# Optimization experiments

Hardware: AMD Instinct MI355X
Metric: run time of the kernel (lower is better)

## Reference

```python
import jax, jax.numpy as jnp
import numpy as np

B, C, H, W = 4, 64, 96, 96
O = 64          # out_channel
K = 9           # 3x3 kernel positions
PAD = 1


def conv3x3(x, w, b):
    # NCHW 3x3 conv, stride 1, pad 1
    y = jax.lax.conv_general_dilated(
        x, w, window_strides=(1, 1), padding=((PAD, PAD), (PAD, PAD)),
        dimension_numbers=("NCHW", "OIHW", "NCHW"))
    return y + b[None, :, None, None]


def deform_conv3x3(x, offset, w, b):
    """torchvision-style DeformConv2d, 3x3, stride 1, pad 1, 1 offset group.
    x: [B, Cin, H, W]; offset: [B, 2*K, H, W] ordered (dy, dx) per kernel pos.
    """
    Bb, Cin, Hh, Ww = x.shape
    off = offset.reshape(Bb, K, 2, Hh, Ww)
    ky, kx = jnp.meshgrid(jnp.arange(3), jnp.arange(3), indexing="ij")
    ky = ky.reshape(K).astype(x.dtype)
    kx = kx.reshape(K).astype(x.dtype)
    hh = jnp.arange(Hh, dtype=x.dtype)
    ww = jnp.arange(Ww, dtype=x.dtype)
    # sampling coords: p0 + p_k + delta_p  -> [B, K, H, W]
    py = hh[None, None, :, None] - PAD + ky[None, :, None, None] + off[:, :, 0]
    px = ww[None, None, None, :] - PAD + kx[None, :, None, None] + off[:, :, 1]

    y0 = jnp.floor(py).astype(jnp.int32)
    x0 = jnp.floor(px).astype(jnp.int32)
    dy = py - y0.astype(x.dtype)
    dx = px - x0.astype(x.dtype)

    x_flat = x.reshape(Bb, Cin, Hh * Ww)

    def gather(yi, xi, wgt):
        valid = ((yi >= 0) & (yi < Hh) & (xi >= 0) & (xi < Ww)).astype(x.dtype)
        idx = (jnp.clip(yi, 0, Hh - 1) * Ww + jnp.clip(xi, 0, Ww - 1)).reshape(Bb, -1)
        vals = jax.vmap(lambda xf, ix: xf[:, ix])(x_flat, idx)  # [B, Cin, K*H*W]
        return vals * (wgt * valid).reshape(Bb, 1, -1)

    sampled = (gather(y0,     x0,     (1 - dy) * (1 - dx))
             + gather(y0,     x0 + 1, (1 - dy) * dx)
             + gather(y0 + 1, x0,     dy * (1 - dx))
             + gather(y0 + 1, x0 + 1, dy * dx))
    sampled = sampled.reshape(Bb, Cin, K, Hh, Ww)
    out = jnp.einsum("bckhw,ock->bohw", sampled, w.reshape(O, Cin, K))
    return out + b[None, :, None, None]


def setup_inputs() -> dict:
    key = jax.random.key(0)
    ks = jax.random.split(key, 6)
    ref_feat = jax.random.normal(ks[0], (B, C, H, W), dtype=jnp.float32)
    dist_feat = jax.random.normal(ks[1], (B, C, H, W), dtype=jnp.float32)
    offset_w = jax.random.normal(ks[2], (2 * K, C, 3, 3), dtype=jnp.float32) * 0.01
    offset_b = jnp.zeros((2 * K,), dtype=jnp.float32)
    deform_w = jax.random.normal(ks[3], (O, 3 * C, 3, 3), dtype=jnp.float32) * 0.05
    deform_b = jax.random.normal(ks[4], (O,), dtype=jnp.float32) * 0.05
    return {"ref_feat": ref_feat, "dist_feat": dist_feat,
            "offset_w": offset_w, "offset_b": offset_b,
            "deform_w": deform_w, "deform_b": deform_b}


def reference(ref_feat, dist_feat, offset_w, offset_b, deform_w, deform_b):
    offset = conv3x3(ref_feat, offset_w, offset_b)
    diff = (ref_feat - dist_feat) ** 2
    feat_in = jnp.concatenate((ref_feat, dist_feat, diff), axis=1)  # [B, 3C, H, W]
    feat = deform_conv3x3(feat_in, offset, deform_w, deform_b)
    feat = jax.nn.relu(feat)
    return (feat, diff)
```

## Files before the change

### kernel.cpp

```cpp
#include <hip/hip_runtime.h>
#include <hip/hip_fp16.h>

#define Wd    96
#define Hd    96
#define HW    9216
#define Bn    4
#define Cn    64
#define C3    192
#define On    64
#define NPIX  (Bn*HW)
#define NFEAT (Bn*Cn*HW)
#define NWTB  (9*6*4*512)
#define NWTB2 (18*2*64*8)
#define NRB3  (Bn*(HW/32))

#define HR    5
#define HC    21
#define HPITCH 400
#define NPR   (HR*HC)

typedef __attribute__((ext_vector_type(8))) short s8v;
typedef __attribute__((ext_vector_type(8))) _Float16 h8v;
typedef __attribute__((ext_vector_type(4))) unsigned int u4v;
typedef __attribute__((ext_vector_type(4))) float f4v;

__device__ __forceinline__ unsigned packh(float lo, float hi) {
    __half2 h = __floats2half2_rn(lo, hi);
    return __builtin_bit_cast(unsigned, h);
}

__global__ __launch_bounds__(256) void repack_wts_kernel(
        const float* __restrict__ ref,
        const float* __restrict__ dist,
        unsigned int* __restrict__ packed,
        float* __restrict__ out_diff,
        const float* __restrict__ dw,
        const float* __restrict__ ow,
        __half* __restrict__ wtb,
        __half* __restrict__ wtb2) {
    __shared__ unsigned lds[96][33];

    int tid = threadIdx.x;

    if (blockIdx.x >= NRB3) {
        int e = (int)(blockIdx.x - NRB3) * 256 + tid;
        if (e < NWTB) {
            int j = e & 7;
            int L = (e >> 3) & 63;
            int mt = (e >> 9) & 3;
            int rest = e >> 11;
            int kc = rest % 6;
            int tap = rest / 6;
            int o = mt * 16 + (L & 15);
            int c = kc * 32 + (L >> 4) * 8 + j;
            wtb[e] = __float2half(dw[((size_t)o * C3 + c) * 9 + tap]);
        } else if (e < NWTB + NWTB2) {
            int e2 = e - NWTB;
            int j = e2 & 7;
            int L = (e2 >> 3) & 63;
            int mt = (e2 >> 9) & 1;
            int kc2 = e2 >> 10;
            int v = mt * 16 + (L & 15);
            int k = kc2 * 32 + ((L >> 4) & 3) * 8 + j;
            int c = k & 63;
            int tap = k >> 6;
            float val = (v < 18) ? ow[((size_t)v * Cn + c) * 9 + tap] : 0.f;
            wtb2[e2] = __float2half(val);
        }
        return;
    }

    int blk = blockIdx.x;
    int b = blk / (HW / 32);
    int pb = (blk - b * (HW / 32)) * 32;
    int pxg = tid & 7;
    int chp = tid >> 3;

    size_t base0 = ((size_t)(b * Cn + 2 * chp)) * HW + pb + pxg * 4;
    size_t base1 = base0 + HW;

    f4v r0 = *(const f4v*)(ref + base0);
    f4v r1 = *(const f4v*)(ref + base1);
    f4v d0 = *(const f4v*)(dist + base0);
    f4v d1 = *(const f4v*)(dist + base1);

    f4v q0 = (r0 - d0) * (r0 - d0);
    f4v q1 = (r1 - d1) * (r1 - d1);
    *(f4v*)(out_diff + base0) = q0;
    *(f4v*)(out_diff + base1) = q1;

#pragma unroll
    for (int j = 0; j < 4; ++j) {
        int p = pxg * 4 + j;
        lds[chp][p]      = packh(r0[j], r1[j]);
        lds[32 + chp][p] = packh(d0[j], d1[j]);
        lds[64 + chp][p] = packh(q0[j], q1[j]);
    }
    __syncthreads();

    unsigned* pko = packed + (size_t)(b * HW + pb) * 96;
#pragma unroll
    for (int k = 0; k < 12; ++k) {
        int i = tid + k * 256;
        int p = i / 96;
        int cp = i - p * 96;
        pko[p * 96 + cp] = lds[cp][p];
    }
}

struct Ctx {
    int o00, o01, o10, o11;
    int l00, l01, l10, l11;
    float W00, W01, W10, W11;
    int inh;
};

__device__ __forceinline__ Ctx mkctx(int t, int y, int x, int xb, float2 o2) {
    Ctx c;
    float py = (float)(y - 1 + t / 3) + o2.x;
    float pxs = (float)(x - 1 + t % 3) + o2.y;
    float fy = floorf(py), fx = floorf(pxs);
    int y0 = (int)fy, x0 = (int)fx;
    int y1 = y0 + 1, x1 = x0 + 1;
    float ay = py - fy, ax = pxs - fx;
    bool vy0 = (unsigned)y0 < (unsigned)Hd;
    bool vy1 = (unsigned)y1 < (unsigned)Hd;
    bool vx0 = (unsigned)x0 < (unsigned)Wd;
    bool vx1 = (unsigned)x1 < (unsigned)Wd;
    c.W00 = (vy0 && vx0) ? (1.f - ay) * (1.f - ax) : 0.f;
    c.W01 = (vy0 && vx1) ? (1.f - ay) * ax : 0.f;
    c.W10 = (vy1 && vx0) ? ay * (1.f - ax) : 0.f;
    c.W11 = (vy1 && vx1) ? ay * ax : 0.f;
    int y0c = min(max(y0, 0), Hd - 1), y1c = min(max(y1, 0), Hd - 1);
    int x0c = min(max(x0, 0), Wd - 1), x1c = min(max(x1, 0), Wd - 1);
    c.o00 = (y0c * Wd + x0c) * (C3 * 2);
    c.o01 = (y0c * Wd + x1c) * (C3 * 2);
    c.o10 = (y1c * Wd + x0c) * (C3 * 2);
    c.o11 = (y1c * Wd + x1c) * (C3 * 2);
    int iy0 = y0c - y + 2, iy1 = y1c - y + 2;
    int ix0 = x0c - xb + 3, ix1 = x1c - xb + 3;
    c.inh = ((unsigned)iy0 < (unsigned)HR) & ((unsigned)iy1 < (unsigned)HR) &
            ((unsigned)ix0 < (unsigned)HC) & ((unsigned)ix1 < (unsigned)HC);
    c.l00 = (iy0 * HC + ix0) * HPITCH;
    c.l01 = (iy0 * HC + ix1) * HPITCH;
    c.l10 = (iy1 * HC + ix0) * HPITCH;
    c.l11 = (iy1 * HC + ix1) * HPITCH;
    return c;
}

__device__ __forceinline__ __half2 uh2(unsigned u) {
    return __builtin_bit_cast(__half2, u);
}

__device__ __forceinline__ void bilin_mfma(const s8v* rw, const Ctx& cc,
        const s8v* __restrict__ Ap, int t, int kb, int L, f4v* acc) {
    __half2 w00 = __float2half2_rn(cc.W00);
    __half2 w01 = __float2half2_rn(cc.W01);
    __half2 w10 = __float2half2_rn(cc.W10);
    __half2 w11 = __float2half2_rn(cc.W11);
#pragma unroll
    for (int i = 0; i < 3; ++i) {
        int kc = kb + i;
        u4v u00 = __builtin_bit_cast(u4v, rw[0 * 3 + i]);
        u4v u01 = __builtin_bit_cast(u4v, rw[1 * 3 + i]);
        u4v u10 = __builtin_bit_cast(u4v, rw[2 * 3 + i]);
        u4v u11 = __builtin_bit_cast(u4v, rw[3 * 3 + i]);
        u4v bu;
#pragma unroll
        for (int p = 0; p < 4; ++p) {
            __half2 v = __hmul2(uh2(u00[p]), w00);
            v = __hfma2(uh2(u01[p]), w01, v);
            v = __hfma2(uh2(u10[p]), w10, v);
            v = __hfma2(uh2(u11[p]), w11, v);
            bu[p] = __builtin_bit_cast(unsigned, v);
        }
        h8v bfrag = __builtin_bit_cast(h8v, bu);
#pragma unroll
        for (int mt = 0; mt < 4; ++mt) {
            h8v a = __builtin_bit_cast(h8v, Ap[((t * 6 + kc) * 4 + mt) * 64 + L]);
            acc[mt] = __builtin_amdgcn_mfma_f32_16x16x32_f16(a, bfrag, acc[mt], 0, 0, 0);
        }
    }
}

__global__ __launch_bounds__(192) void fused_mfma(
        const __half* __restrict__ packed,
        const __half* __restrict__ wtb2,
        const float* __restrict__ ob,
        const __half* __restrict__ wtb,
        const float* __restrict__ db,
        float* __restrict__ out) {
    __shared__ f4v halo[NPR * (HPITCH / 16)];
    __shared__ float red[2][64 * 17];
    __shared__ float off_lds[16][18];

    int tid = threadIdx.x;
    int L = tid & 63;
    int wv = tid / 64;
    int px = L & 15;
    int lg = L >> 4;
    int blk = blockIdx.x;
    int region = (blk & 7) * 288 + (blk >> 3);
    int p0 = region * 16;
    int b = p0 / HW;
    int pb = p0 - b * HW;
    int yb = pb / Wd;
    int xb = pb - yb * Wd;
    int x = xb + px, y = yb;
    int tbase = wv * 3;

    const char* pkb = (const char*)packed + (size_t)b * HW * (C3 * 2);
    const char* hb = (const char*)halo;

#pragma unroll 1
    for (int i = tid; i < NPR * 24; i += 192) {
        int pr = i / 24;
        int ck = i - pr * 24;
        int iy = pr / HC, ix = pr - iy * HC;
        int gy = min(max(yb - 2 + iy, 0), Hd - 1);
        int gx = min(max(xb - 3 + ix, 0), Wd - 1);
        halo[pr * (HPITCH / 16) + ck] =
            *(const f4v*)(pkb + ((size_t)(gy * Wd + gx)) * (C3 * 2) + ck * 16);
    }
    __syncthreads();

    {
        const s8v* Ap = (const s8v*)wtb2;
        f4v acc0 = {0.f, 0.f, 0.f, 0.f};
        f4v acc1 = {0.f, 0.f, 0.f, 0.f};
#pragma unroll
        for (int tt = 0; tt < 3; ++tt) {
            int t = tbase + tt;
            int ty = t / 3, tx = t - ty * 3;
            int yy = y - 1 + ty, xx = x - 1 + tx;
            bool val = (unsigned)yy < (unsigned)Hd && (unsigned)xx < (unsigned)Wd;
            short m = val ? (short)-1 : (short)0;
            int lofs = ((1 + ty) * HC + (px + 2 + tx)) * HPITCH + lg * 16;
#pragma unroll
            for (int kc = 0; kc < 2; ++kc) {
                s8v braw = *(const s8v*)(hb + lofs + kc * 64) & m;
                h8v bfrag = __builtin_bit_cast(h8v, braw);
                h8v a0 = __builtin_bit_cast(h8v, Ap[((t * 2 + kc) * 2 + 0) * 64 + L]);
                h8v a1 = __builtin_bit_cast(h8v, Ap[((t * 2 + kc) * 2 + 1) * 64 + L]);
                acc0 = __builtin_amdgcn_mfma_f32_16x16x32_f16(a0, bfrag, acc0, 0, 0, 0);
                acc1 = __builtin_amdgcn_mfma_f32_16x16x32_f16(a1, bfrag, acc1, 0, 0, 0);
            }
        }
        if (wv != 0) {
            float* r = red[wv - 1] + L * 9;
#pragma unroll
            for (int i = 0; i < 4; ++i) r[i] = acc0[i];
#pragma unroll
            for (int i = 0; i < 4; ++i) r[4 + i] = acc1[i];
        }
        __syncthreads();
        if (wv == 0) {
            const float* r0 = red[0] + L * 9;
            const float* r1 = red[1] + L * 9;
#pragma unroll
            for (int r = 0; r < 4; ++r) {
                int v = lg * 4 + r;
                off_lds[px][v] = acc0[r] + r0[r] + r1[r] + ob[v];
            }
            if (lg == 0) {
#pragma unroll
                for (int r = 0; r < 2; ++r)
                    off_lds[px][16 + r] = acc1[r] + r0[4 + r] + r1[4 + r] + ob[16 + r];
            }
        }
        __syncthreads();
    }

    const s8v* Ap = (const s8v*)wtb;

    Ctx ctx[3];
    int ok = 1;
#pragma unroll
    for (int tt = 0; tt < 3; ++tt) {
        int t = tbase + tt;
        float2 o2 = {off_lds[px][2 * t], off_lds[px][2 * t + 1]};
        ctx[tt] = mkctx(t, y, x, xb, o2);
        ok &= ctx[tt].inh;
    }

    f4v acc[4];
    acc[0] = acc[1] = acc[2] = acc[3] = (f4v){0.f, 0.f, 0.f, 0.f};

    if (__all(ok)) {
#pragma unroll
        for (int h = 0; h < 6; ++h) {
            int tt = h >> 1;
            int t = tbase + tt;
            int kb = (h & 1) * 3;
            const Ctx cc = ctx[tt];
            s8v rw[12];
#pragma unroll
            for (int i = 0; i < 3; ++i) {
                int co = ((kb + i) * 4 + lg) * 16;
                rw[0 * 3 + i] = *(const s8v*)(hb + cc.l00 + co);
                rw[1 * 3 + i] = *(const s8v*)(hb + cc.l01 + co);
                rw[2 * 3 + i] = *(const s8v*)(hb + cc.l10 + co);
                rw[3 * 3 + i] = *(const s8v*)(hb + cc.l11 + co);
            }
            bilin_mfma(rw, cc, Ap, t, kb, L, acc);
        }
    } else {
#pragma unroll
        for (int h = 0; h < 6; ++h) {
            int tt = h >> 1;
            int t = tbase + tt;
            int kb = (h & 1) * 3;
            const Ctx cc = ctx[tt];
            s8v rw[12];
#pragma unroll
            for (int i = 0; i < 3; ++i) {
                int co = ((kb + i) * 4 + lg) * 16;
                rw[0 * 3 + i] = *(const s8v*)(pkb + cc.o00 + co);
                rw[1 * 3 + i] = *(const s8v*)(pkb + cc.o01 + co);
                rw[2 * 3 + i] = *(const s8v*)(pkb + cc.o10 + co);
                rw[3 * 3 + i] = *(const s8v*)(pkb + cc.o11 + co);
            }
            bilin_mfma(rw, cc, Ap, t, kb, L, acc);
        }
    }

    if (wv != 0) {
        float* r = red[wv - 1] + L * 17;
#pragma unroll
        for (int mt = 0; mt < 4; ++mt)
#pragma unroll
            for (int q = 0; q < 4; ++q)
                r[mt * 4 + q] = acc[mt][q];
    }
    __syncthreads();
    if (wv == 0) {
        const float* r0 = red[0] + L * 17;
        const float* r1 = red[1] + L * 17;
#pragma unroll
        for (int mt = 0; mt < 4; ++mt) {
#pragma unroll
            for (int q = 0; q < 4; ++q) {
                int o = mt * 16 + lg * 4 + q;
                float v = acc[mt][q] + r0[mt * 4 + q] + r1[mt * 4 + q] + db[o];
                out[((size_t)(b * On + o)) * HW + pb + px] = fmaxf(v, 0.f);
            }
        }
    }
}

extern "C" void kernel_launch(void* const* d_in, const int* in_sizes, int n_in,
                              void* d_out, int out_size, void* d_ws, size_t ws_size,
                              hipStream_t stream) {
    const float* ref  = (const float*)d_in[0];
    const float* dist = (const float*)d_in[1];
    const float* ow   = (const float*)d_in[2];
    const float* ob   = (const float*)d_in[3];
    const float* dw   = (const float*)d_in[4];
    const float* db   = (const float*)d_in[5];

    float* out = (float*)d_out;

    __half* ws_wtb  = (__half*)d_ws;
    __half* ws_wtb2 = ws_wtb + NWTB;
    __half* ws_pk   = ws_wtb2 + NWTB2;

    int wts_blocks = (NWTB + NWTB2 + 255) / 256;
    repack_wts_kernel<<<NRB3 + wts_blocks, 256, 0, stream>>>(
        ref, dist, (unsigned int*)ws_pk, out + NFEAT, dw, ow, ws_wtb, ws_wtb2);
    fused_mfma<<<NPIX / 16, 192, 0, stream>>>(
        ws_pk, ws_wtb2, ob, ws_wtb, db, out);
}
```

Baseline: 120.7 us.

## Process two output rows per block sharing a taller halo tile

Each block now covers a 2x16 pixel tile with 384 threads (two groups of three waves) instead of one row of 16 pixels with 192 threads. The LDS halo grows from 5 to 6 rows and is shared by both rows, which cuts redundant halo loads per output pixel. The halo load is restructured to issue all global loads into registers before writing to LDS, and the final reduction buffer aliases the halo region, which needs an extra barrier. The larger LDS footprint and block size may reduce occupancy.

```diff
diff --git a/kernel.cpp b/kernel.cpp
--- a/kernel.cpp
+++ b/kernel.cpp
@@ -14,10 +14,14 @@
 #define NWTB2 (18*2*64*8)
 #define NRB3  (Bn*(HW/32))
 
-#define HR    5
+#define HR2   6
 #define HC    21
 #define HPITCH 400
-#define NPR   (HR*HC)
+#define NPR2  (HR2*HC)
+#define SELEM (NPR2*24)
+#define HALO_B (NPR2*HPITCH)
+#define REDA_B (2*2*64*9*4)
+#define NFBLK 1152
 
 typedef __attribute__((ext_vector_type(8))) short s8v;
 typedef __attribute__((ext_vector_type(8))) _Float16 h8v;
@@ -115,7 +119,8 @@
     int inh;
 };
 
-__device__ __forceinline__ Ctx mkctx(int t, int y, int x, int xb, float2 o2) {
+__device__ __forceinline__ Ctx mkctx(int t, int y, int x, int xb, int yb,
+                                     float2 o2) {
     Ctx c;
     float py = (float)(y - 1 + t / 3) + o2.x;
     float pxs = (float)(x - 1 + t % 3) + o2.y;
@@ -137,9 +142,9 @@
     c.o01 = (y0c * Wd + x1c) * (C3 * 2);
     c.o10 = (y1c * Wd + x0c) * (C3 * 2);
     c.o11 = (y1c * Wd + x1c) * (C3 * 2);
-    int iy0 = y0c - y + 2, iy1 = y1c - y + 2;
+    int iy0 = y0c - yb + 2, iy1 = y1c - yb + 2;
     int ix0 = x0c - xb + 3, ix1 = x1c - xb + 3;
-    c.inh = ((unsigned)iy0 < (unsigned)HR) & ((unsigned)iy1 < (unsigned)HR) &
+    c.inh = ((unsigned)iy0 < (unsigned)HR2) & ((unsigned)iy1 < (unsigned)HR2) &
             ((unsigned)ix0 < (unsigned)HC) & ((unsigned)ix1 < (unsigned)HC);
     c.l00 = (iy0 * HC + ix0) * HPITCH;
     c.l01 = (iy0 * HC + ix1) * HPITCH;
@@ -183,44 +188,58 @@
     }
 }
 
-__global__ __launch_bounds__(192) void fused_mfma(
+__global__ __launch_bounds__(384, 3) void fused_mfma(
         const __half* __restrict__ packed,
         const __half* __restrict__ wtb2,
         const float* __restrict__ ob,
         const __half* __restrict__ wtb,
         const float* __restrict__ db,
         float* __restrict__ out) {
-    __shared__ f4v halo[NPR * (HPITCH / 16)];
-    __shared__ float red[2][64 * 17];
-    __shared__ float off_lds[16][18];
+    __shared__ __align__(16) char smem[HALO_B + REDA_B + 2 * 16 * 18 * 4];
+    f4v* halo = (f4v*)smem;
+    float* redA = (float*)(smem + HALO_B);
+    float (*off_l)[18] = (float(*)[18])(smem + HALO_B + REDA_B);
+    float* redB = (float*)smem;
 
     int tid = threadIdx.x;
     int L = tid & 63;
-    int wv = tid / 64;
+    int wv = tid >> 6;
+    int g  = wv / 3;
+    int kv = wv - g * 3;
     int px = L & 15;
     int lg = L >> 4;
     int blk = blockIdx.x;
-    int region = (blk & 7) * 288 + (blk >> 3);
-    int p0 = region * 16;
-    int b = p0 / HW;
-    int pb = p0 - b * HW;
-    int yb = pb / Wd;
-    int xb = pb - yb * Wd;
-    int x = xb + px, y = yb;
-    int tbase = wv * 3;
+    int region = (blk & 7) * 144 + (blk >> 3);
+    int b = region / 288;
+    int rt = region - b * 288;
+    int yt = rt / 6;
+    int xt = rt - yt * 6;
+    int yb = yt * 2, xb = xt * 16;
+    int y = yb + g, x = xb + px;
+    int pb = y * Wd + xb;
+    int tbase = kv * 3;
 
     const char* pkb = (const char*)packed + (size_t)b * HW * (C3 * 2);
     const char* hb = (const char*)halo;
 
-#pragma unroll 1
-    for (int i = tid; i < NPR * 24; i += 192) {
-        int pr = i / 24;
-        int ck = i - pr * 24;
-        int iy = pr / HC, ix = pr - iy * HC;
-        int gy = min(max(yb - 2 + iy, 0), Hd - 1);
-        int gx = min(max(xb - 3 + ix, 0), Wd - 1);
-        halo[pr * (HPITCH / 16) + ck] =
-            *(const f4v*)(pkb + ((size_t)(gy * Wd + gx)) * (C3 * 2) + ck * 16);
+    {
+        f4v stg[8];
+        int slot[8];
+#pragma unroll
+        for (int k = 0; k < 8; ++k) {
+            int i = tid + k * 384;
+            bool act = (k < 7) ? true : (tid < SELEM - 7 * 384);
+            int pr = i / 24, ck = i - pr * 24;
+            int iy = pr / HC, ix = pr - iy * HC;
+            int gy = min(max(yb - 2 + iy, 0), Hd - 1);
+            int gx = min(max(xb - 3 + ix, 0), Wd - 1);
+            slot[k] = act ? (pr * (HPITCH / 16) + ck) : -1;
+            if (act)
+                stg[k] = *(const f4v*)(pkb + ((size_t)(gy * Wd + gx)) * (C3 * 2) + ck * 16);
+        }
+#pragma unroll
+        for (int k = 0; k < 8; ++k)
+            if (slot[k] >= 0) halo[slot[k]] = stg[k];
     }
     __syncthreads();
 
@@ -235,7 +254,7 @@
             int yy = y - 1 + ty, xx = x - 1 + tx;
             bool val = (unsigned)yy < (unsigned)Hd && (unsigned)xx < (unsigned)Wd;
             short m = val ? (short)-1 : (short)0;
-            int lofs = ((1 + ty) * HC + (px + 2 + tx)) * HPITCH + lg * 16;
+            int lofs = ((g + 1 + ty) * HC + (px + 2 + tx)) * HPITCH + lg * 16;
 #pragma unroll
             for (int kc = 0; kc < 2; ++kc) {
                 s8v braw = *(const s8v*)(hb + lofs + kc * 64) & m;
@@ -246,26 +265,26 @@
                 acc1 = __builtin_amdgcn_mfma_f32_16x16x32_f16(a1, bfrag, acc1, 0, 0, 0);
             }
         }
-        if (wv != 0) {
-            float* r = red[wv - 1] + L * 9;
+        if (kv != 0) {
+            float* r = redA + ((g * 2 + kv - 1) * 64 + L) * 9;
 #pragma unroll
             for (int i = 0; i < 4; ++i) r[i] = acc0[i];
 #pragma unroll
             for (int i = 0; i < 4; ++i) r[4 + i] = acc1[i];
         }
         __syncthreads();
-        if (wv == 0) {
-            const float* r0 = red[0] + L * 9;
-            const float* r1 = red[1] + L * 9;
+        if (kv == 0) {
+            const float* r0 = redA + ((g * 2 + 0) * 64 + L) * 9;
+            const float* r1 = redA + ((g * 2 + 1) * 64 + L) * 9;
 #pragma unroll
             for (int r = 0; r < 4; ++r) {
                 int v = lg * 4 + r;
-                off_lds[px][v] = acc0[r] + r0[r] + r1[r] + ob[v];
+                off_l[g * 16 + px][v] = acc0[r] + r0[r] + r1[r] + ob[v];
             }
             if (lg == 0) {
 #pragma unroll
                 for (int r = 0; r < 2; ++r)
-                    off_lds[px][16 + r] = acc1[r] + r0[4 + r] + r1[4 + r] + ob[16 + r];
+                    off_l[g * 16 + px][16 + r] = acc1[r] + r0[4 + r] + r1[4 + r] + ob[16 + r];
             }
         }
         __syncthreads();
@@ -278,8 +297,8 @@
 #pragma unroll
     for (int tt = 0; tt < 3; ++tt) {
         int t = tbase + tt;
-        float2 o2 = {off_lds[px][2 * t], off_lds[px][2 * t + 1]};
-        ctx[tt] = mkctx(t, y, x, xb, o2);
+        float2 o2 = {off_l[g * 16 + px][2 * t], off_l[g * 16 + px][2 * t + 1]};
+        ctx[tt] = mkctx(t, y, x, xb, yb, o2);
         ok &= ctx[tt].inh;
     }
 
@@ -324,8 +343,9 @@
         }
     }
 
-    if (wv != 0) {
-        float* r = red[wv - 1] + L * 17;
+    __syncthreads();
+    if (kv != 0) {
+        float* r = redB + ((g * 2 + kv - 1) * 64 + L) * 17;
 #pragma unroll
         for (int mt = 0; mt < 4; ++mt)
 #pragma unroll
@@ -333,9 +353,9 @@
                 r[mt * 4 + q] = acc[mt][q];
     }
     __syncthreads();
-    if (wv == 0) {
-        const float* r0 = red[0] + L * 17;
-        const float* r1 = red[1] + L * 17;
+    if (kv == 0) {
+        const float* r0 = redB + ((g * 2 + 0) * 64 + L) * 17;
+        const float* r1 = redB + ((g * 2 + 1) * 64 + L) * 17;
 #pragma unroll
         for (int mt = 0; mt < 4; ++mt) {
 #pragma unroll
@@ -367,6 +387,6 @@
     int wts_blocks = (NWTB + NWTB2 + 255) / 256;
     repack_wts_kernel<<<NRB3 + wts_blocks, 256, 0, stream>>>(
         ref, dist, (unsigned int*)ws_pk, out + NFEAT, dw, ow, ws_wtb, ws_wtb2);
-    fused_mfma<<<NPIX / 16, 192, 0, stream>>>(
+    fused_mfma<<<NFBLK, 384, 0, stream>>>(
         ws_pk, ws_wtb2, ob, ws_wtb, db, out);
 }
```

After: 119.2 us. No clear change (-1.2%).
